# Kernel tuning notes

Measured on AMD Instinct MI355X. Metric: run time of the kernel, lower is better.

## Reference

```python
import jax, jax.numpy as jnp
from jax import lax
import numpy as np

CONF_THRES = 0.55
IOU_THRES = 0.45
MAX_DET = 1000
MAX_WH = 7680.0   # class offset for class-aware NMS (agnostic=False)
K = 4096          # NMS candidate cap (yolov5 max_nms analogue, jit-static)
IMG = 640         # letterboxed network input size
B, N, NC = 16, 25200, 80


def setup_inputs() -> dict:
    key = jax.random.key(0)
    k1, k2, k3, k4 = jax.random.split(key, 4)
    cxcy = jax.random.uniform(k1, (B, N, 2), jnp.float32, 0.0, IMG)
    wh = jax.random.uniform(k2, (B, N, 2), jnp.float32, 2.0, 120.0)
    obj = jax.random.uniform(k3, (B, N, 1), jnp.float32) ** 4
    cls = jax.random.uniform(k4, (B, N, NC), jnp.float32)
    pred = jnp.concatenate([cxcy, wh, obj, cls], axis=-1)  # [B, N, 5+NC]
    return {"pred": pred, "img0_h": 1080, "img0_w": 1920}


def xywh2xyxy(x):
    cx, cy, w, h = x[..., 0], x[..., 1], x[..., 2], x[..., 3]
    return jnp.stack([cx - w / 2, cy - h / 2, cx + w / 2, cy + h / 2], axis=-1)


def box_iou(a, b):
    # a: [K,4], b: [K,4] xyxy -> [K,K]
    lt = jnp.maximum(a[:, None, :2], b[None, :, :2])
    rb = jnp.minimum(a[:, None, 2:], b[None, :, 2:])
    wh = jnp.clip(rb - lt, 0.0)
    inter = wh[..., 0] * wh[..., 1]
    area_a = (a[:, 2] - a[:, 0]) * (a[:, 3] - a[:, 1])
    area_b = (b[:, 2] - b[:, 0]) * (b[:, 3] - b[:, 1])
    return inter / (area_a[:, None] + area_b[None, :] - inter + 1e-7)


def _nms_image(p, img0_h, img0_w):
    # p: [N, 5+NC]
    obj = p[:, 4]
    cls_conf = p[:, 5:] * obj[:, None]          # conf = obj * cls
    conf = cls_conf.max(axis=-1)
    cls_id = cls_conf.argmax(axis=-1)
    valid = (obj > CONF_THRES) & (conf > CONF_THRES)
    score = jnp.where(valid, conf, -1.0)
    # top-K candidates, sorted by confidence (descending)
    top_scores, top_idx = lax.top_k(score, K)
    boxes = xywh2xyxy(p[top_idx, :4])           # [K,4]
    cl = cls_id[top_idx].astype(p.dtype)        # [K]
    iou = box_iou(boxes + cl[:, None] * MAX_WH, boxes + cl[:, None] * MAX_WH)
    idx = jnp.arange(K)
    keep0 = top_scores > 0.0

    def body(i, keep):
        # suppress i if a higher-scoring kept box overlaps it too much
        sup = jnp.any(keep & (idx < i) & (iou[:, i] > IOU_THRES))
        return keep.at[i].set(keep[i] & ~sup)

    keep = lax.fori_loop(0, K, body, keep0)
    kept_score = jnp.where(keep, top_scores, -1.0)
    fs, fi = lax.top_k(kept_score, MAX_DET)
    fb = boxes[fi]                              # [MAX_DET,4]
    fc = cl[fi]
    fvalid = fs > 0.0
    # scale_boxes: letterboxed 640x640 -> original img0
    gain = min(IMG / img0_h, IMG / img0_w)
    pad_x = (IMG - img0_w * gain) / 2
    pad_y = (IMG - img0_h * gain) / 2
    fb = (fb - jnp.array([pad_x, pad_y, pad_x, pad_y], fb.dtype)) / gain
    fb = jnp.clip(fb, 0.0, jnp.array([img0_w, img0_h, img0_w, img0_h], fb.dtype))
    fb = jnp.round(fb)
    det = jnp.concatenate([fb, fs[:, None], fc[:, None]], axis=-1)  # [MAX_DET,6]
    return jnp.where(fvalid[:, None], det, 0.0)


def reference(pred, img0_h, img0_w):
    return jax.vmap(lambda p: _nms_image(p, img0_h, img0_w))(pred)
```

## Files before the change

### kernel.cpp

```cpp
#include <hip/hip_runtime.h>

#define BB 16
#define NN 25200
#define NC 80
#define ROWL 85
#define KTOP 4096
#define MAXDET 1000
#define CONF_T 0.55f
#define IOU_T 0.45f
#define MAX_WH_F 7680.0f
#define CNT_STRIDE 32
#define PCNT_STRIDE 4
#define CCAP 256
#define NBIN 2048

#define OFF_CNT   20480
#define OFF_KCNT  22528
#define OFF_BUCK  24576
#define OFF_KEPT  2646016
#define ZERO_WORDS 6144

__global__ void zero_kernel(unsigned int* __restrict__ w) {
  w[blockIdx.x * 256 + threadIdx.x] = 0u;
}

__global__ __launch_bounds__(256) void score_kernel(const float* __restrict__ pred,
                             unsigned long long* __restrict__ buckets,
                             unsigned int* __restrict__ pcnt,
                             unsigned int* __restrict__ cnt) {
  const int b = blockIdx.y;
  const int lane = threadIdx.x & 63;
  const int w = threadIdx.x >> 6;
  const int g = lane >> 4;
  const int gl = lane & 15;
  const float* __restrict__ pb = pred + (size_t)b * NN * ROWL;
  unsigned int nvacc = 0;
  for (int t = 0; t < 4; ++t) {
    const int seg = blockIdx.x * 16 + w * 4 + t;
    const int a0 = seg * 64;
    if (a0 >= NN) break;
    const int a = a0 + lane;
    float obj = 0.0f;
    if (a < NN) obj = pb[(size_t)a * ROWL + 4];
    unsigned long long mask = __ballot(obj > CONF_T);
    while (mask) {
      int s0 = __ffsll(mask) - 1; mask &= mask - 1;
      int s1 = -1, s2 = -1, s3 = -1;
      if (mask) { s1 = __ffsll(mask) - 1; mask &= mask - 1; }
      if (mask) { s2 = __ffsll(mask) - 1; mask &= mask - 1; }
      if (mask) { s3 = __ffsll(mask) - 1; mask &= mask - 1; }
      const int sg = (g == 0) ? s0 : (g == 1) ? s1 : (g == 2) ? s2 : s3;
      const bool act = (sg >= 0);
      const int srow = act ? sg : s0;
      const int aa = a0 + srow;
      const float objg = __shfl(obj, srow, 64);
      const float* __restrict__ row = pb + (size_t)aa * ROWL;
      float best = -1.0f; int bi = gl;
      #pragma unroll
      for (int u = 0; u < 5; ++u) {
        float v = row[5 + gl + 16 * u] * objg;
        if (v > best) { best = v; bi = gl + 16 * u; }
      }
      #pragma unroll
      for (int off = 1; off <= 8; off <<= 1) {
        float ov = __shfl_xor(best, off, 64);
        int oi = __shfl_xor(bi, off, 64);
        if (ov > best || (ov == best && oi < bi)) { best = ov; bi = oi; }
      }
      bool emit = act && (gl == 0) && (best > CONF_T);
      if (emit) {
        unsigned long long key =
            ((unsigned long long)__float_as_uint(best) << 32) |
            ((unsigned long long)((~(unsigned)aa) & 0xFFFFu) << 16) |
            (unsigned long long)(unsigned)bi;
        unsigned int slot = atomicAdd(&pcnt[(b * NC + bi) * PCNT_STRIDE], 1u);
        if (slot < CCAP)
          buckets[((size_t)(b * NC + bi) << 8) + slot] = key;
      }
      unsigned long long em = __ballot(emit);
      if (lane == 0) nvacc += (unsigned int)__popcll(em);
    }
  }
  if (lane == 0 && nvacc)
    atomicAdd(&cnt[b * CNT_STRIDE], nvacc);
}

__device__ __forceinline__ bool iou_sup(float ax1, float ay1, float ax2, float ay2,
                                        float aar, float bx1, float by1, float bx2,
                                        float by2, float bar) {
  float ltx = fmaxf(ax1, bx1), lty = fmaxf(ay1, by1);
  float rbx = fminf(ax2, bx2), rby = fminf(ay2, by2);
  float wv = rbx - ltx; wv = wv > 0.0f ? wv : 0.0f;
  float hv = rby - lty; hv = hv > 0.0f ? hv : 0.0f;
  float inter = wv * hv;
  float iou = inter / (aar + bar - inter + 1e-7f);
  return iou > IOU_T;
}

__global__ __launch_bounds__(256) void class_nms_kernel(
    const float* __restrict__ pred,
    const unsigned long long* __restrict__ buckets,
    const unsigned int* __restrict__ pcnt,
    const unsigned int* __restrict__ cnt,
    unsigned long long* __restrict__ kept,
    unsigned int* __restrict__ kcnt) {
  const int c = blockIdx.x * 4 + (threadIdx.x >> 6);
  const int b = blockIdx.y;
  const int lane = threadIdx.x & 63;
  unsigned int pc = pcnt[(b * NC + c) * PCNT_STRIDE];
  int n_c = (int)(pc < (unsigned)CCAP ? pc : (unsigned)CCAP);
  const unsigned long long* __restrict__ bk = buckets + ((size_t)(b * NC + c) << 8);
  const float* __restrict__ pb = pred + (size_t)b * NN * ROWL;
  const float offc = (float)c * MAX_WH_F;
  const int count = (int)cnt[b * CNT_STRIDE];

  if (n_c == 0) return;

  if (n_c <= 64 && count <= KTOP) {
    unsigned long long v0 = (lane < n_c) ? bk[lane] : 0ull;
    for (int k2 = 2; k2 <= 64; k2 <<= 1) {
      for (int j = k2 >> 1; j >= 1; j >>= 1) {
        unsigned long long vo = __shfl_xor(v0, j, 64);
        bool desc = ((lane & k2) == 0);
        bool low = ((lane & j) == 0);
        if ((desc == low) ? (vo > v0) : (vo < v0)) v0 = vo;
      }
    }
    float x1 = 0.f, y1 = 0.f, x2 = 0.f, y2 = 0.f, aar = 0.f;
    const bool inr = (lane < n_c);
    if (inr) {
      unsigned int lo = (unsigned int)v0;
      int aa = (int)((~(lo >> 16)) & 0xFFFFu);
      const float* row = pb + (size_t)aa * ROWL;
      float cx = row[0], cy = row[1], w2 = row[2], h2 = row[3];
      x1 = (cx - w2 / 2.0f) + offc;
      y1 = (cy - h2 / 2.0f) + offc;
      x2 = (cx + w2 / 2.0f) + offc;
      y2 = (cy + h2 / 2.0f) + offc;
      aar = (x2 - x1) * (y2 - y1);
    }
    unsigned long long rowreg = 0ull;
    for (int i2 = 0; i2 < n_c; ++i2) {
      float bx1 = __shfl(x1, i2, 64), by1 = __shfl(y1, i2, 64);
      float bx2 = __shfl(x2, i2, 64), by2 = __shfl(y2, i2, 64);
      float bar = __shfl(aar, i2, 64);
      bool sup = inr && (lane > i2) &&
                 iou_sup(bx1, by1, bx2, by2, bar, x1, y1, x2, y2, aar);
      unsigned long long rm = __ballot(sup);
      if (lane == i2) rowreg = rm;
    }
    unsigned long long cand = (n_c >= 64) ? ~0ull : ((1ull << n_c) - 1ull);
    unsigned long long keepm = 0ull;
    while (cand) {
      int i = __ffsll(cand) - 1;
      keepm |= (1ull << i);
      unsigned long long rowi = __shfl(rowreg, i, 64);
      cand &= ~rowi;
      cand &= ~(1ull << i);
    }
    int keep0 = (int)((keepm >> lane) & 1ull);
    unsigned long long m0 = __ballot(keep0 != 0);
    int tot = (int)__popcll(m0);
    unsigned int base3 = 0;
    if (lane == 0) base3 = atomicAdd(&kcnt[b * CNT_STRIDE], (unsigned int)tot);
    base3 = (unsigned int)__shfl((int)base3, 0, 64);
    if (keep0) {
      unsigned int slot = base3 + (unsigned int)__popcll(m0 & ((1ull << lane) - 1ull));
      if (slot < (unsigned)KTOP) kept[(size_t)b * KTOP + slot] = v0;
    }
    return;
  }

  unsigned long long v[4];
  #pragma unroll
  for (int r = 0; r < 4; ++r) {
    int e = (r << 6) + lane;
    v[r] = (e < n_c) ? bk[e] : 0ull;
  }
  if (count > KTOP) {
    unsigned long long T = 0ull;
    for (int bit = 63; bit >= 0; --bit) {
      unsigned long long T2 = T | (1ull << bit);
      int cge = 0;
      for (int c2 = 0; c2 < NC; ++c2) {
        unsigned int p2 = pcnt[(b * NC + c2) * PCNT_STRIDE];
        int n2 = (int)(p2 < (unsigned)CCAP ? p2 : (unsigned)CCAP);
        const unsigned long long* bk2 = buckets + ((size_t)(b * NC + c2) << 8);
        for (int base2 = 0; base2 < n2; base2 += 64) {
          int i = base2 + lane;
          bool ge = (i < n2) && (bk2[i] >= T2);
          cge += (int)__popcll(__ballot(ge));
        }
      }
      if (cge >= KTOP) T = T2;
    }
    #pragma unroll
    for (int r = 0; r < 4; ++r) if (v[r] < T) v[r] = 0ull;
    n_c = 0;
    #pragma unroll
    for (int r = 0; r < 4; ++r) n_c += (int)__popcll(__ballot(v[r] != 0ull));
    if (n_c == 0) return;
  }
  for (int k2 = 2; k2 <= 256; k2 <<= 1) {
    if (k2 == 256) {
      #pragma unroll
      for (int r = 0; r < 2; ++r) {
        unsigned e = (unsigned)((r << 6) + lane);
        bool desc = ((e & k2) == 0);
        unsigned long long lo_ = v[r], hi_ = v[r + 2];
        bool sw = desc ? (lo_ < hi_) : (lo_ > hi_);
        v[r] = sw ? hi_ : lo_; v[r + 2] = sw ? lo_ : hi_;
      }
    }
    if (k2 >= 128) {
      #pragma unroll
      for (int rr = 0; rr < 2; ++rr) {
        int r = rr * 2;
        unsigned e = (unsigned)((r << 6) + lane);
        bool desc = ((e & k2) == 0);
        unsigned long long lo_ = v[r], hi_ = v[r + 1];
        bool sw = desc ? (lo_ < hi_) : (lo_ > hi_);
        v[r] = sw ? hi_ : lo_; v[r + 1] = sw ? lo_ : hi_;
      }
    }
    int j0 = (k2 >> 1) < 32 ? (k2 >> 1) : 32;
    for (int j = j0; j >= 1; j >>= 1) {
      #pragma unroll
      for (int r = 0; r < 4; ++r) {
        unsigned e = (unsigned)((r << 6) + lane);
        unsigned long long vo = __shfl_xor(v[r], j, 64);
        bool desc = ((e & k2) == 0);
        bool low = ((e & j) == 0);
        if ((desc == low) ? (vo > v[r]) : (vo < v[r])) v[r] = vo;
      }
    }
  }
  float x1r[4], y1r[4], x2r[4], y2r[4], ar[4];
  int keepr[4];
  #pragma unroll
  for (int r = 0; r < 4; ++r) {
    int e = (r << 6) + lane;
    keepr[r] = 0; x1r[r] = 0.f; y1r[r] = 0.f; x2r[r] = 0.f; y2r[r] = 0.f; ar[r] = 0.f;
    if (e < n_c) {
      unsigned int lo = (unsigned int)v[r];
      int aa = (int)((~(lo >> 16)) & 0xFFFFu);
      const float* row = pb + (size_t)aa * ROWL;
      float cx = row[0], cy = row[1], w2 = row[2], h2 = row[3];
      x1r[r] = (cx - w2 / 2.0f) + offc;
      y1r[r] = (cy - h2 / 2.0f) + offc;
      x2r[r] = (cx + w2 / 2.0f) + offc;
      y2r[r] = (cy + h2 / 2.0f) + offc;
      ar[r] = (x2r[r] - x1r[r]) * (y2r[r] - y1r[r]);
      keepr[r] = 1;
    }
  }
  for (int i2 = 0; i2 < n_c; ++i2) {
    int ci = i2 >> 6, li = i2 & 63;
    int ki; float bx1v, by1v, bx2v, by2v, bav;
    #define BCAST(R) { ki = __shfl(keepr[R], li, 64); bx1v = __shfl(x1r[R], li, 64); \
                       by1v = __shfl(y1r[R], li, 64); bx2v = __shfl(x2r[R], li, 64); \
                       by2v = __shfl(y2r[R], li, 64); bav = __shfl(ar[R], li, 64); }
    switch (ci) {
      case 0: BCAST(0); break;
      case 1: BCAST(1); break;
      case 2: BCAST(2); break;
      default: BCAST(3); break;
    }
    #undef BCAST
    if (!ki) continue;
    #pragma unroll
    for (int r = 0; r < 4; ++r) {
      int e = (r << 6) + lane;
      if (keepr[r] && e > i2 &&
          iou_sup(bx1v, by1v, bx2v, by2v, bav, x1r[r], y1r[r], x2r[r], y2r[r], ar[r]))
        keepr[r] = 0;
    }
  }
  unsigned long long m[4];
  int tot = 0;
  #pragma unroll
  for (int r = 0; r < 4; ++r) {
    m[r] = __ballot(keepr[r] != 0);
    tot += (int)__popcll(m[r]);
  }
  unsigned int base3 = 0;
  if (lane == 0) base3 = atomicAdd(&kcnt[b * CNT_STRIDE], (unsigned int)tot);
  base3 = (unsigned int)__shfl((int)base3, 0, 64);
  unsigned int start = base3;
  #pragma unroll
  for (int r = 0; r < 4; ++r) {
    if (keepr[r]) {
      unsigned int slot = start + (unsigned int)__popcll(m[r] & ((1ull << lane) - 1ull));
      if (slot < (unsigned)KTOP) kept[(size_t)b * KTOP + slot] = v[r];
    }
    start += (unsigned int)__popcll(m[r]);
  }
}

__global__ __launch_bounds__(1024) void finalize_kernel(
    const float* __restrict__ pred,
    const unsigned long long* __restrict__ kept,
    const unsigned int* __restrict__ kcnt,
    const int* __restrict__ ihp, const int* __restrict__ iwp,
    float* __restrict__ out) {
  __shared__ unsigned int hist[NBIN];
  __shared__ unsigned int sufx[NBIN];
  __shared__ unsigned int curs[NBIN];
  __shared__ unsigned int wsum[16], woff[16];
  __shared__ unsigned long long skey[KTOP];
  const int b = blockIdx.x;
  const int tid = threadIdx.x;
  const int lane = tid & 63;
  const int w = tid >> 6;
  unsigned int kcr = kcnt[b * CNT_STRIDE];
  const int kc = (int)(kcr < (unsigned)KTOP ? kcr : (unsigned)KTOP);
  const unsigned long long* __restrict__ kb = kept + (size_t)b * KTOP;

  hist[2 * tid] = 0u; hist[2 * tid + 1] = 0u;
  __syncthreads();

  unsigned long long myk[4];
  int myb[4];
  #pragma unroll
  for (int r = 0; r < 4; ++r) {
    int i = tid + (r << 10);
    myb[r] = -1; myk[r] = 0ull;
    if (i < kc) {
      unsigned long long k = kb[i];
      int bin = (int)((k >> 44) & (unsigned long long)(NBIN - 1));
      myk[r] = k; myb[r] = bin;
      atomicAdd(&hist[bin], 1u);
    }
  }
  __syncthreads();

  unsigned int h0 = hist[2 * tid], h1 = hist[2 * tid + 1];
  unsigned int v = h0 + h1;
  #pragma unroll
  for (int off = 1; off < 64; off <<= 1) {
    unsigned int o = __shfl_down(v, off, 64);
    if (lane + off < 64) v += o;
  }
  if (lane == 0) wsum[w] = v;
  __syncthreads();
  if (tid < 16) {
    unsigned int s = 0;
    for (int j = tid + 1; j < 16; ++j) s += wsum[j];
    woff[tid] = s;
  }
  __syncthreads();
  unsigned int incl = v + woff[w];
  unsigned int excl = incl - (h0 + h1);
  sufx[2 * tid] = excl + h1;
  sufx[2 * tid + 1] = excl;
  curs[2 * tid] = excl + h1;
  curs[2 * tid + 1] = excl;
  __syncthreads();

  #pragma unroll
  for (int r = 0; r < 4; ++r) {
    if (myb[r] >= 0) {
      unsigned int p = atomicAdd(&curs[myb[r]], 1u);
      skey[p] = myk[r];
    }
  }
  __syncthreads();

  const int h = ihp[0], w3 = iwp[0];
  const double gd = fmin(640.0 / (double)h, 640.0 / (double)w3);
  const float gain = (float)gd;
  const float padx = (float)((640.0 - (double)w3 * gd) * 0.5);
  const float pady = (float)((640.0 - (double)h * gd) * 0.5);
  const float wf = (float)w3, hf = (float)h;
  #pragma unroll
  for (int r = 0; r < 4; ++r) {
    if (myb[r] >= 0) {
      unsigned long long k = myk[r];
      unsigned int gstart = sufx[myb[r]];
      unsigned int gcnt = hist[myb[r]];
      unsigned int rank = gstart;
      for (unsigned int j = 0; j < gcnt; ++j)
        rank += (skey[gstart + j] > k) ? 1u : 0u;
      if (rank < MAXDET) {
        unsigned int lo = (unsigned int)k;
        int aa = (int)((~(lo >> 16)) & 0xFFFFu);
        int cls = (int)(lo & 0xFFFFu);
        float score = __uint_as_float((unsigned int)(k >> 32));
        const float* row = pred + ((size_t)b * NN + aa) * ROWL;
        float cx = row[0], cy = row[1], wd = row[2], ht = row[3];
        float x1 = cx - wd / 2.0f, y1 = cy - ht / 2.0f;
        float x2 = cx + wd / 2.0f, y2 = cy + ht / 2.0f;
        x1 = rintf(fminf(fmaxf((x1 - padx) / gain, 0.0f), wf));
        y1 = rintf(fminf(fmaxf((y1 - pady) / gain, 0.0f), hf));
        x2 = rintf(fminf(fmaxf((x2 - padx) / gain, 0.0f), wf));
        y2 = rintf(fminf(fmaxf((y2 - pady) / gain, 0.0f), hf));
        float* o = out + ((size_t)b * MAXDET + (int)rank) * 6;
        o[0] = x1; o[1] = y1; o[2] = x2; o[3] = y2;
        o[4] = score; o[5] = (float)cls;
      }
    }
  }
  for (int i = kc + tid; i < MAXDET; i += 1024) {
    float* o = out + ((size_t)b * MAXDET + i) * 6;
    o[0] = 0.0f; o[1] = 0.0f; o[2] = 0.0f; o[3] = 0.0f; o[4] = 0.0f; o[5] = 0.0f;
  }
}

extern "C" void kernel_launch(void* const* d_in, const int* in_sizes, int n_in,
                              void* d_out, int out_size, void* d_ws, size_t ws_size,
                              hipStream_t stream) {
  const float* pred = (const float*)d_in[0];
  const int* ih = (const int*)d_in[1];
  const int* iw = (const int*)d_in[2];
  float* out = (float*)d_out;
  char* ws = (char*)d_ws;

  unsigned int* pcnt = (unsigned int*)ws;
  unsigned int* cnt = (unsigned int*)(ws + OFF_CNT);
  unsigned int* kcnt = (unsigned int*)(ws + OFF_KCNT);
  unsigned long long* buckets = (unsigned long long*)(ws + OFF_BUCK);
  unsigned long long* kept = (unsigned long long*)(ws + OFF_KEPT);

  zero_kernel<<<ZERO_WORDS / 256, 256, 0, stream>>>((unsigned int*)ws);
  dim3 sgrid(25, BB);
  score_kernel<<<sgrid, 256, 0, stream>>>(pred, buckets, pcnt, cnt);
  dim3 cgrid(NC / 4, BB);
  class_nms_kernel<<<cgrid, 256, 0, stream>>>(pred, buckets, pcnt, cnt, kept, kcnt);
  finalize_kernel<<<BB, 1024, 0, stream>>>(pred, kept, kcnt, ih, iw, out);
}
```

Before: 82.16 us.

## Fuse per-class NMS into finalize kernel and widen score kernel grid

Merges the per-class NMS kernel into the finalize kernel. Each of 16 wavefronts in a 1024-thread block now processes 5 classes and writes kept keys to shared memory, so the global kept buffer, its counter and one kernel launch go away. The score kernel now gives each wavefront a single 64-anchor segment over a larger grid instead of looping over 4 segments. Per-class counters are spaced further apart to reduce atomic contention. The trade-off is that NMS now runs on only 16 blocks, serialising 5 classes per wavefront and reducing parallelism.

```diff
diff --git a/kernel.cpp b/kernel.cpp
--- a/kernel.cpp
+++ b/kernel.cpp
@@ -10,15 +10,13 @@
 #define IOU_T 0.45f
 #define MAX_WH_F 7680.0f
 #define CNT_STRIDE 32
-#define PCNT_STRIDE 4
+#define PCNT_STRIDE 16
 #define CCAP 256
 #define NBIN 2048
 
-#define OFF_CNT   20480
-#define OFF_KCNT  22528
-#define OFF_BUCK  24576
-#define OFF_KEPT  2646016
-#define ZERO_WORDS 6144
+#define OFF_CNT   81920
+#define OFF_BUCK  86016
+#define ZERO_WORDS 21504
 
 __global__ void zero_kernel(unsigned int* __restrict__ w) {
   w[blockIdx.x * 256 + threadIdx.x] = 0u;
@@ -30,56 +28,51 @@
                              unsigned int* __restrict__ cnt) {
   const int b = blockIdx.y;
   const int lane = threadIdx.x & 63;
-  const int w = threadIdx.x >> 6;
+  const int a0 = blockIdx.x * 256 + (threadIdx.x & ~63);
+  const int a = a0 + lane;
   const int g = lane >> 4;
   const int gl = lane & 15;
   const float* __restrict__ pb = pred + (size_t)b * NN * ROWL;
+  float obj = 0.0f;
+  if (a < NN) obj = pb[(size_t)a * ROWL + 4];
+  unsigned long long mask = __ballot(obj > CONF_T);
   unsigned int nvacc = 0;
-  for (int t = 0; t < 4; ++t) {
-    const int seg = blockIdx.x * 16 + w * 4 + t;
-    const int a0 = seg * 64;
-    if (a0 >= NN) break;
-    const int a = a0 + lane;
-    float obj = 0.0f;
-    if (a < NN) obj = pb[(size_t)a * ROWL + 4];
-    unsigned long long mask = __ballot(obj > CONF_T);
-    while (mask) {
-      int s0 = __ffsll(mask) - 1; mask &= mask - 1;
-      int s1 = -1, s2 = -1, s3 = -1;
-      if (mask) { s1 = __ffsll(mask) - 1; mask &= mask - 1; }
-      if (mask) { s2 = __ffsll(mask) - 1; mask &= mask - 1; }
-      if (mask) { s3 = __ffsll(mask) - 1; mask &= mask - 1; }
-      const int sg = (g == 0) ? s0 : (g == 1) ? s1 : (g == 2) ? s2 : s3;
-      const bool act = (sg >= 0);
-      const int srow = act ? sg : s0;
-      const int aa = a0 + srow;
-      const float objg = __shfl(obj, srow, 64);
-      const float* __restrict__ row = pb + (size_t)aa * ROWL;
-      float best = -1.0f; int bi = gl;
-      #pragma unroll
-      for (int u = 0; u < 5; ++u) {
-        float v = row[5 + gl + 16 * u] * objg;
-        if (v > best) { best = v; bi = gl + 16 * u; }
-      }
-      #pragma unroll
-      for (int off = 1; off <= 8; off <<= 1) {
-        float ov = __shfl_xor(best, off, 64);
-        int oi = __shfl_xor(bi, off, 64);
-        if (ov > best || (ov == best && oi < bi)) { best = ov; bi = oi; }
-      }
-      bool emit = act && (gl == 0) && (best > CONF_T);
-      if (emit) {
-        unsigned long long key =
-            ((unsigned long long)__float_as_uint(best) << 32) |
-            ((unsigned long long)((~(unsigned)aa) & 0xFFFFu) << 16) |
-            (unsigned long long)(unsigned)bi;
-        unsigned int slot = atomicAdd(&pcnt[(b * NC + bi) * PCNT_STRIDE], 1u);
-        if (slot < CCAP)
-          buckets[((size_t)(b * NC + bi) << 8) + slot] = key;
-      }
-      unsigned long long em = __ballot(emit);
-      if (lane == 0) nvacc += (unsigned int)__popcll(em);
-    }
+  while (mask) {
+    int s0 = __ffsll(mask) - 1; mask &= mask - 1;
+    int s1 = -1, s2 = -1, s3 = -1;
+    if (mask) { s1 = __ffsll(mask) - 1; mask &= mask - 1; }
+    if (mask) { s2 = __ffsll(mask) - 1; mask &= mask - 1; }
+    if (mask) { s3 = __ffsll(mask) - 1; mask &= mask - 1; }
+    const int sg = (g == 0) ? s0 : (g == 1) ? s1 : (g == 2) ? s2 : s3;
+    const bool act = (sg >= 0);
+    const int srow = act ? sg : s0;
+    const int aa = a0 + srow;
+    const float objg = __shfl(obj, srow, 64);
+    const float* __restrict__ row = pb + (size_t)aa * ROWL;
+    float best = -1.0f; int bi = gl;
+    #pragma unroll
+    for (int t = 0; t < 5; ++t) {
+      float v = row[5 + gl + 16 * t] * objg;
+      if (v > best) { best = v; bi = gl + 16 * t; }
+    }
+    #pragma unroll
+    for (int off = 1; off <= 8; off <<= 1) {
+      float ov = __shfl_xor(best, off, 64);
+      int oi = __shfl_xor(bi, off, 64);
+      if (ov > best || (ov == best && oi < bi)) { best = ov; bi = oi; }
+    }
+    bool emit = act && (gl == 0) && (best > CONF_T);
+    if (emit) {
+      unsigned long long key =
+          ((unsigned long long)__float_as_uint(best) << 32) |
+          ((unsigned long long)((~(unsigned)aa) & 0xFFFFu) << 16) |
+          (unsigned long long)(unsigned)bi;
+      unsigned int slot = atomicAdd(&pcnt[(b * NC + bi) * PCNT_STRIDE], 1u);
+      if (slot < CCAP)
+        buckets[((size_t)(b * NC + bi) << 8) + slot] = key;
+    }
+    unsigned long long em = __ballot(emit);
+    if (lane == 0) nvacc += (unsigned int)__popcll(em);
   }
   if (lane == 0 && nvacc)
     atomicAdd(&cnt[b * CNT_STRIDE], nvacc);
@@ -97,225 +90,229 @@
   return iou > IOU_T;
 }
 
-__global__ __launch_bounds__(256) void class_nms_kernel(
+__global__ __launch_bounds__(1024) void nms_finalize_kernel(
     const float* __restrict__ pred,
     const unsigned long long* __restrict__ buckets,
     const unsigned int* __restrict__ pcnt,
     const unsigned int* __restrict__ cnt,
-    unsigned long long* __restrict__ kept,
-    unsigned int* __restrict__ kcnt) {
-  const int c = blockIdx.x * 4 + (threadIdx.x >> 6);
-  const int b = blockIdx.y;
-  const int lane = threadIdx.x & 63;
-  unsigned int pc = pcnt[(b * NC + c) * PCNT_STRIDE];
-  int n_c = (int)(pc < (unsigned)CCAP ? pc : (unsigned)CCAP);
-  const unsigned long long* __restrict__ bk = buckets + ((size_t)(b * NC + c) << 8);
-  const float* __restrict__ pb = pred + (size_t)b * NN * ROWL;
-  const float offc = (float)c * MAX_WH_F;
-  const int count = (int)cnt[b * CNT_STRIDE];
-
-  if (n_c == 0) return;
-
-  if (n_c <= 64 && count <= KTOP) {
-    unsigned long long v0 = (lane < n_c) ? bk[lane] : 0ull;
-    for (int k2 = 2; k2 <= 64; k2 <<= 1) {
-      for (int j = k2 >> 1; j >= 1; j >>= 1) {
-        unsigned long long vo = __shfl_xor(v0, j, 64);
-        bool desc = ((lane & k2) == 0);
-        bool low = ((lane & j) == 0);
-        if ((desc == low) ? (vo > v0) : (vo < v0)) v0 = vo;
-      }
-    }
-    float x1 = 0.f, y1 = 0.f, x2 = 0.f, y2 = 0.f, aar = 0.f;
-    const bool inr = (lane < n_c);
-    if (inr) {
-      unsigned int lo = (unsigned int)v0;
-      int aa = (int)((~(lo >> 16)) & 0xFFFFu);
-      const float* row = pb + (size_t)aa * ROWL;
-      float cx = row[0], cy = row[1], w2 = row[2], h2 = row[3];
-      x1 = (cx - w2 / 2.0f) + offc;
-      y1 = (cy - h2 / 2.0f) + offc;
-      x2 = (cx + w2 / 2.0f) + offc;
-      y2 = (cy + h2 / 2.0f) + offc;
-      aar = (x2 - x1) * (y2 - y1);
-    }
-    unsigned long long rowreg = 0ull;
-    for (int i2 = 0; i2 < n_c; ++i2) {
-      float bx1 = __shfl(x1, i2, 64), by1 = __shfl(y1, i2, 64);
-      float bx2 = __shfl(x2, i2, 64), by2 = __shfl(y2, i2, 64);
-      float bar = __shfl(aar, i2, 64);
-      bool sup = inr && (lane > i2) &&
-                 iou_sup(bx1, by1, bx2, by2, bar, x1, y1, x2, y2, aar);
-      unsigned long long rm = __ballot(sup);
-      if (lane == i2) rowreg = rm;
-    }
-    unsigned long long cand = (n_c >= 64) ? ~0ull : ((1ull << n_c) - 1ull);
-    unsigned long long keepm = 0ull;
-    while (cand) {
-      int i = __ffsll(cand) - 1;
-      keepm |= (1ull << i);
-      unsigned long long rowi = __shfl(rowreg, i, 64);
-      cand &= ~rowi;
-      cand &= ~(1ull << i);
-    }
-    int keep0 = (int)((keepm >> lane) & 1ull);
-    unsigned long long m0 = __ballot(keep0 != 0);
-    int tot = (int)__popcll(m0);
-    unsigned int base3 = 0;
-    if (lane == 0) base3 = atomicAdd(&kcnt[b * CNT_STRIDE], (unsigned int)tot);
-    base3 = (unsigned int)__shfl((int)base3, 0, 64);
-    if (keep0) {
-      unsigned int slot = base3 + (unsigned int)__popcll(m0 & ((1ull << lane) - 1ull));
-      if (slot < (unsigned)KTOP) kept[(size_t)b * KTOP + slot] = v0;
-    }
-    return;
-  }
-
-  unsigned long long v[4];
-  #pragma unroll
-  for (int r = 0; r < 4; ++r) {
-    int e = (r << 6) + lane;
-    v[r] = (e < n_c) ? bk[e] : 0ull;
-  }
-  if (count > KTOP) {
-    unsigned long long T = 0ull;
-    for (int bit = 63; bit >= 0; --bit) {
-      unsigned long long T2 = T | (1ull << bit);
-      int cge = 0;
-      for (int c2 = 0; c2 < NC; ++c2) {
-        unsigned int p2 = pcnt[(b * NC + c2) * PCNT_STRIDE];
-        int n2 = (int)(p2 < (unsigned)CCAP ? p2 : (unsigned)CCAP);
-        const unsigned long long* bk2 = buckets + ((size_t)(b * NC + c2) << 8);
-        for (int base2 = 0; base2 < n2; base2 += 64) {
-          int i = base2 + lane;
-          bool ge = (i < n2) && (bk2[i] >= T2);
-          cge += (int)__popcll(__ballot(ge));
-        }
-      }
-      if (cge >= KTOP) T = T2;
-    }
-    #pragma unroll
-    for (int r = 0; r < 4; ++r) if (v[r] < T) v[r] = 0ull;
-    n_c = 0;
-    #pragma unroll
-    for (int r = 0; r < 4; ++r) n_c += (int)__popcll(__ballot(v[r] != 0ull));
-    if (n_c == 0) return;
-  }
-  for (int k2 = 2; k2 <= 256; k2 <<= 1) {
-    if (k2 == 256) {
-      #pragma unroll
-      for (int r = 0; r < 2; ++r) {
-        unsigned e = (unsigned)((r << 6) + lane);
-        bool desc = ((e & k2) == 0);
-        unsigned long long lo_ = v[r], hi_ = v[r + 2];
-        bool sw = desc ? (lo_ < hi_) : (lo_ > hi_);
-        v[r] = sw ? hi_ : lo_; v[r + 2] = sw ? lo_ : hi_;
-      }
-    }
-    if (k2 >= 128) {
-      #pragma unroll
-      for (int rr = 0; rr < 2; ++rr) {
-        int r = rr * 2;
-        unsigned e = (unsigned)((r << 6) + lane);
-        bool desc = ((e & k2) == 0);
-        unsigned long long lo_ = v[r], hi_ = v[r + 1];
-        bool sw = desc ? (lo_ < hi_) : (lo_ > hi_);
-        v[r] = sw ? hi_ : lo_; v[r + 1] = sw ? lo_ : hi_;
-      }
-    }
-    int j0 = (k2 >> 1) < 32 ? (k2 >> 1) : 32;
-    for (int j = j0; j >= 1; j >>= 1) {
-      #pragma unroll
-      for (int r = 0; r < 4; ++r) {
-        unsigned e = (unsigned)((r << 6) + lane);
-        unsigned long long vo = __shfl_xor(v[r], j, 64);
-        bool desc = ((e & k2) == 0);
-        bool low = ((e & j) == 0);
-        if ((desc == low) ? (vo > v[r]) : (vo < v[r])) v[r] = vo;
-      }
-    }
-  }
-  float x1r[4], y1r[4], x2r[4], y2r[4], ar[4];
-  int keepr[4];
-  #pragma unroll
-  for (int r = 0; r < 4; ++r) {
-    int e = (r << 6) + lane;
-    keepr[r] = 0; x1r[r] = 0.f; y1r[r] = 0.f; x2r[r] = 0.f; y2r[r] = 0.f; ar[r] = 0.f;
-    if (e < n_c) {
-      unsigned int lo = (unsigned int)v[r];
-      int aa = (int)((~(lo >> 16)) & 0xFFFFu);
-      const float* row = pb + (size_t)aa * ROWL;
-      float cx = row[0], cy = row[1], w2 = row[2], h2 = row[3];
-      x1r[r] = (cx - w2 / 2.0f) + offc;
-      y1r[r] = (cy - h2 / 2.0f) + offc;
-      x2r[r] = (cx + w2 / 2.0f) + offc;
-      y2r[r] = (cy + h2 / 2.0f) + offc;
-      ar[r] = (x2r[r] - x1r[r]) * (y2r[r] - y1r[r]);
-      keepr[r] = 1;
-    }
-  }
-  for (int i2 = 0; i2 < n_c; ++i2) {
-    int ci = i2 >> 6, li = i2 & 63;
-    int ki; float bx1v, by1v, bx2v, by2v, bav;
-    #define BCAST(R) { ki = __shfl(keepr[R], li, 64); bx1v = __shfl(x1r[R], li, 64); \
-                       by1v = __shfl(y1r[R], li, 64); bx2v = __shfl(x2r[R], li, 64); \
-                       by2v = __shfl(y2r[R], li, 64); bav = __shfl(ar[R], li, 64); }
-    switch (ci) {
-      case 0: BCAST(0); break;
-      case 1: BCAST(1); break;
-      case 2: BCAST(2); break;
-      default: BCAST(3); break;
-    }
-    #undef BCAST
-    if (!ki) continue;
-    #pragma unroll
-    for (int r = 0; r < 4; ++r) {
-      int e = (r << 6) + lane;
-      if (keepr[r] && e > i2 &&
-          iou_sup(bx1v, by1v, bx2v, by2v, bav, x1r[r], y1r[r], x2r[r], y2r[r], ar[r]))
-        keepr[r] = 0;
-    }
-  }
-  unsigned long long m[4];
-  int tot = 0;
-  #pragma unroll
-  for (int r = 0; r < 4; ++r) {
-    m[r] = __ballot(keepr[r] != 0);
-    tot += (int)__popcll(m[r]);
-  }
-  unsigned int base3 = 0;
-  if (lane == 0) base3 = atomicAdd(&kcnt[b * CNT_STRIDE], (unsigned int)tot);
-  base3 = (unsigned int)__shfl((int)base3, 0, 64);
-  unsigned int start = base3;
-  #pragma unroll
-  for (int r = 0; r < 4; ++r) {
-    if (keepr[r]) {
-      unsigned int slot = start + (unsigned int)__popcll(m[r] & ((1ull << lane) - 1ull));
-      if (slot < (unsigned)KTOP) kept[(size_t)b * KTOP + slot] = v[r];
-    }
-    start += (unsigned int)__popcll(m[r]);
-  }
-}
-
-__global__ __launch_bounds__(1024) void finalize_kernel(
-    const float* __restrict__ pred,
-    const unsigned long long* __restrict__ kept,
-    const unsigned int* __restrict__ kcnt,
     const int* __restrict__ ihp, const int* __restrict__ iwp,
     float* __restrict__ out) {
+  __shared__ unsigned long long vkeys[KTOP];
   __shared__ unsigned int hist[NBIN];
   __shared__ unsigned int sufx[NBIN];
   __shared__ unsigned int curs[NBIN];
+  __shared__ unsigned long long skey[KTOP];
   __shared__ unsigned int wsum[16], woff[16];
-  __shared__ unsigned long long skey[KTOP];
+  __shared__ unsigned int kcnt;
   const int b = blockIdx.x;
   const int tid = threadIdx.x;
   const int lane = tid & 63;
   const int w = tid >> 6;
-  unsigned int kcr = kcnt[b * CNT_STRIDE];
-  const int kc = (int)(kcr < (unsigned)KTOP ? kcr : (unsigned)KTOP);
-  const unsigned long long* __restrict__ kb = kept + (size_t)b * KTOP;
-
+  const float* __restrict__ pb = pred + (size_t)b * NN * ROWL;
+  const int count = (int)cnt[b * CNT_STRIDE];
+  if (tid == 0) kcnt = 0u;
+  __syncthreads();
+
+  unsigned int pcv[5];
+  unsigned long long vpre[5];
+  #pragma unroll
+  for (int cc = 0; cc < 5; ++cc) {
+    const int c = w + (cc << 4);
+    pcv[cc] = pcnt[(b * NC + c) * PCNT_STRIDE];
+    vpre[cc] = buckets[((size_t)(b * NC + c) << 8) + lane];
+  }
+
+  #pragma unroll 1
+  for (int cc = 0; cc < 5; ++cc) {
+    const int c = w + (cc << 4);
+    int n_c = (int)(pcv[cc] < (unsigned)CCAP ? pcv[cc] : (unsigned)CCAP);
+    if (n_c == 0) continue;
+    const unsigned long long* __restrict__ bkc = buckets + ((size_t)(b * NC + c) << 8);
+    const float offc = (float)c * MAX_WH_F;
+
+    if (n_c <= 64 && count <= KTOP) {
+      unsigned long long v0 = vpre[cc];
+      if (lane >= n_c) v0 = 0ull;
+      for (int k2 = 2; k2 <= 64; k2 <<= 1) {
+        for (int j = k2 >> 1; j >= 1; j >>= 1) {
+          unsigned long long vo = __shfl_xor(v0, j, 64);
+          bool desc = ((lane & k2) == 0);
+          bool low = ((lane & j) == 0);
+          if ((desc == low) ? (vo > v0) : (vo < v0)) v0 = vo;
+        }
+      }
+      float x1 = 0.f, y1 = 0.f, x2 = 0.f, y2 = 0.f, aar = 0.f;
+      const bool inr = (lane < n_c);
+      if (inr) {
+        unsigned int lo = (unsigned int)v0;
+        int aa = (int)((~(lo >> 16)) & 0xFFFFu);
+        const float* row = pb + (size_t)aa * ROWL;
+        float cx = row[0], cy = row[1], w2 = row[2], h2 = row[3];
+        x1 = (cx - w2 / 2.0f) + offc;
+        y1 = (cy - h2 / 2.0f) + offc;
+        x2 = (cx + w2 / 2.0f) + offc;
+        y2 = (cy + h2 / 2.0f) + offc;
+        aar = (x2 - x1) * (y2 - y1);
+      }
+      unsigned long long rowreg = 0ull;
+      for (int i2 = 0; i2 < n_c; ++i2) {
+        float bx1 = __shfl(x1, i2, 64), by1 = __shfl(y1, i2, 64);
+        float bx2 = __shfl(x2, i2, 64), by2 = __shfl(y2, i2, 64);
+        float bar = __shfl(aar, i2, 64);
+        bool sup = inr && (lane > i2) &&
+                   iou_sup(bx1, by1, bx2, by2, bar, x1, y1, x2, y2, aar);
+        unsigned long long rm = __ballot(sup);
+        if (lane == i2) rowreg = rm;
+      }
+      unsigned long long cand = (n_c >= 64) ? ~0ull : ((1ull << n_c) - 1ull);
+      unsigned long long keepm = 0ull;
+      while (cand) {
+        int i = __ffsll(cand) - 1;
+        keepm |= (1ull << i);
+        unsigned long long rowi = __shfl(rowreg, i, 64);
+        cand &= ~rowi;
+        cand &= ~(1ull << i);
+      }
+      int keep0 = (int)((keepm >> lane) & 1ull);
+      unsigned long long m0 = __ballot(keep0 != 0);
+      int tot = (int)__popcll(m0);
+      unsigned int base3 = 0;
+      if (lane == 0) base3 = atomicAdd(&kcnt, (unsigned int)tot);
+      base3 = (unsigned int)__shfl((int)base3, 0, 64);
+      if (keep0) {
+        unsigned int slot = base3 + (unsigned int)__popcll(m0 & ((1ull << lane) - 1ull));
+        if (slot < (unsigned)KTOP) vkeys[slot] = v0;
+      }
+    } else {
+      unsigned long long v[4];
+      #pragma unroll
+      for (int r = 0; r < 4; ++r) {
+        int e = (r << 6) + lane;
+        v[r] = (e < n_c) ? bkc[e] : 0ull;
+      }
+      if (count > KTOP) {
+        unsigned long long T = 0ull;
+        for (int bit = 63; bit >= 0; --bit) {
+          unsigned long long T2 = T | (1ull << bit);
+          int cge = 0;
+          for (int c2 = 0; c2 < NC; ++c2) {
+            unsigned int p2 = pcnt[(b * NC + c2) * PCNT_STRIDE];
+            int n2 = (int)(p2 < (unsigned)CCAP ? p2 : (unsigned)CCAP);
+            const unsigned long long* bk2 = buckets + ((size_t)(b * NC + c2) << 8);
+            for (int base2 = 0; base2 < n2; base2 += 64) {
+              int i = base2 + lane;
+              bool ge = (i < n2) && (bk2[i] >= T2);
+              cge += (int)__popcll(__ballot(ge));
+            }
+          }
+          if (cge >= KTOP) T = T2;
+        }
+        #pragma unroll
+        for (int r = 0; r < 4; ++r) if (v[r] < T) v[r] = 0ull;
+        n_c = 0;
+        #pragma unroll
+        for (int r = 0; r < 4; ++r) n_c += (int)__popcll(__ballot(v[r] != 0ull));
+        if (n_c == 0) continue;
+      }
+      for (int k2 = 2; k2 <= 256; k2 <<= 1) {
+        if (k2 == 256) {
+          #pragma unroll
+          for (int r = 0; r < 2; ++r) {
+            unsigned e = (unsigned)((r << 6) + lane);
+            bool desc = ((e & k2) == 0);
+            unsigned long long lo_ = v[r], hi_ = v[r + 2];
+            bool sw = desc ? (lo_ < hi_) : (lo_ > hi_);
+            v[r] = sw ? hi_ : lo_; v[r + 2] = sw ? lo_ : hi_;
+          }
+        }
+        if (k2 >= 128) {
+          #pragma unroll
+          for (int rr = 0; rr < 2; ++rr) {
+            int r = rr * 2;
+            unsigned e = (unsigned)((r << 6) + lane);
+            bool desc = ((e & k2) == 0);
+            unsigned long long lo_ = v[r], hi_ = v[r + 1];
+            bool sw = desc ? (lo_ < hi_) : (lo_ > hi_);
+            v[r] = sw ? hi_ : lo_; v[r + 1] = sw ? lo_ : hi_;
+          }
+        }
+        int j0 = (k2 >> 1) < 32 ? (k2 >> 1) : 32;
+        for (int j = j0; j >= 1; j >>= 1) {
+          #pragma unroll
+          for (int r = 0; r < 4; ++r) {
+            unsigned e = (unsigned)((r << 6) + lane);
+            unsigned long long vo = __shfl_xor(v[r], j, 64);
+            bool desc = ((e & k2) == 0);
+            bool low = ((e & j) == 0);
+            if ((desc == low) ? (vo > v[r]) : (vo < v[r])) v[r] = vo;
+          }
+        }
+      }
+      float x1r[4], y1r[4], x2r[4], y2r[4], ar[4];
+      int keepr[4];
+      #pragma unroll
+      for (int r = 0; r < 4; ++r) {
+        int e = (r << 6) + lane;
+        keepr[r] = 0; x1r[r] = 0.f; y1r[r] = 0.f; x2r[r] = 0.f; y2r[r] = 0.f; ar[r] = 0.f;
+        if (e < n_c) {
+          unsigned int lo = (unsigned int)v[r];
+          int aa = (int)((~(lo >> 16)) & 0xFFFFu);
+          const float* row = pb + (size_t)aa * ROWL;
+          float cx = row[0], cy = row[1], w2 = row[2], h2 = row[3];
+          x1r[r] = (cx - w2 / 2.0f) + offc;
+          y1r[r] = (cy - h2 / 2.0f) + offc;
+          x2r[r] = (cx + w2 / 2.0f) + offc;
+          y2r[r] = (cy + h2 / 2.0f) + offc;
+          ar[r] = (x2r[r] - x1r[r]) * (y2r[r] - y1r[r]);
+          keepr[r] = 1;
+        }
+      }
+      for (int i2 = 0; i2 < n_c; ++i2) {
+        int ci = i2 >> 6, li = i2 & 63;
+        int ki; float bx1v, by1v, bx2v, by2v, bav;
+        #define BCAST(R) { ki = __shfl(keepr[R], li, 64); bx1v = __shfl(x1r[R], li, 64); \
+                           by1v = __shfl(y1r[R], li, 64); bx2v = __shfl(x2r[R], li, 64); \
+                           by2v = __shfl(y2r[R], li, 64); bav = __shfl(ar[R], li, 64); }
+        switch (ci) {
+          case 0: BCAST(0); break;
+          case 1: BCAST(1); break;
+          case 2: BCAST(2); break;
+          default: BCAST(3); break;
+        }
+        #undef BCAST
+        if (!ki) continue;
+        #pragma unroll
+        for (int r = 0; r < 4; ++r) {
+          int e = (r << 6) + lane;
+          if (keepr[r] && e > i2 &&
+              iou_sup(bx1v, by1v, bx2v, by2v, bav, x1r[r], y1r[r], x2r[r], y2r[r], ar[r]))
+            keepr[r] = 0;
+        }
+      }
+      unsigned long long m[4];
+      int tot = 0;
+      #pragma unroll
+      for (int r = 0; r < 4; ++r) {
+        m[r] = __ballot(keepr[r] != 0);
+        tot += (int)__popcll(m[r]);
+      }
+      unsigned int base3 = 0;
+      if (lane == 0) base3 = atomicAdd(&kcnt, (unsigned int)tot);
+      base3 = (unsigned int)__shfl((int)base3, 0, 64);
+      unsigned int start = base3;
+      #pragma unroll
+      for (int r = 0; r < 4; ++r) {
+        if (keepr[r]) {
+          unsigned int slot = start + (unsigned int)__popcll(m[r] & ((1ull << lane) - 1ull));
+          if (slot < (unsigned)KTOP) vkeys[slot] = v[r];
+        }
+        start += (unsigned int)__popcll(m[r]);
+      }
+    }
+  }
+  __syncthreads();
+
+  const int kc = (int)(kcnt < (unsigned)KTOP ? kcnt : (unsigned)KTOP);
   hist[2 * tid] = 0u; hist[2 * tid + 1] = 0u;
   __syncthreads();
 
@@ -326,7 +323,7 @@
     int i = tid + (r << 10);
     myb[r] = -1; myk[r] = 0ull;
     if (i < kc) {
-      unsigned long long k = kb[i];
+      unsigned long long k = vkeys[i];
       int bin = (int)((k >> 44) & (unsigned long long)(NBIN - 1));
       myk[r] = k; myb[r] = bin;
       atomicAdd(&hist[bin], 1u);
@@ -386,7 +383,7 @@
         int aa = (int)((~(lo >> 16)) & 0xFFFFu);
         int cls = (int)(lo & 0xFFFFu);
         float score = __uint_as_float((unsigned int)(k >> 32));
-        const float* row = pred + ((size_t)b * NN + aa) * ROWL;
+        const float* row = pb + (size_t)aa * ROWL;
         float cx = row[0], cy = row[1], wd = row[2], ht = row[3];
         float x1 = cx - wd / 2.0f, y1 = cy - ht / 2.0f;
         float x2 = cx + wd / 2.0f, y2 = cy + ht / 2.0f;
@@ -417,14 +414,10 @@
 
   unsigned int* pcnt = (unsigned int*)ws;
   unsigned int* cnt = (unsigned int*)(ws + OFF_CNT);
-  unsigned int* kcnt = (unsigned int*)(ws + OFF_KCNT);
   unsigned long long* buckets = (unsigned long long*)(ws + OFF_BUCK);
-  unsigned long long* kept = (unsigned long long*)(ws + OFF_KEPT);
 
   zero_kernel<<<ZERO_WORDS / 256, 256, 0, stream>>>((unsigned int*)ws);
-  dim3 sgrid(25, BB);
+  dim3 sgrid((NN + 255) / 256, BB);
   score_kernel<<<sgrid, 256, 0, stream>>>(pred, buckets, pcnt, cnt);
-  dim3 cgrid(NC / 4, BB);
-  class_nms_kernel<<<cgrid, 256, 0, stream>>>(pred, buckets, pcnt, cnt, kept, kcnt);
-  finalize_kernel<<<BB, 1024, 0, stream>>>(pred, kept, kcnt, ih, iw, out);
+  nms_finalize_kernel<<<BB, 1024, 0, stream>>>(pred, buckets, pcnt, cnt, ih, iw, out);
 }
```

Result: slower. 159.4 us (+94.0%).
